# Optimization experiments

Measured on AMD Instinct MI355X. Metric: run time of the kernel, lower is better.

The kernel has to match this reference:

```python
import jax, jax.numpy as jnp
import numpy as np

N = 50000      # nodes
E = 800000     # edges (before self loops)
HID = 128      # hidden_dim
FEAT = 128     # feat_dim
NEG_SLOPE = 0.2
BN_EPS = 1e-5


def setup_inputs() -> dict:
    key = jax.random.key(0)
    ks = jax.random.split(key, 16)
    s = lambda d: 1.0 / np.sqrt(d).astype(np.float32)
    return {
        "x": jax.random.normal(ks[0], (N, HID), jnp.float32),
        "edge_index": jax.random.randint(ks[1], (2, E), 0, N, jnp.int32),
        # GATConv 1 (hidden -> hidden)
        "W1": jax.random.normal(ks[2], (HID, HID), jnp.float32) * s(HID),
        "att_src1": jax.random.normal(ks[3], (HID,), jnp.float32) * s(HID),
        "att_dst1": jax.random.normal(ks[4], (HID,), jnp.float32) * s(HID),
        "b1": jnp.zeros((HID,), jnp.float32),
        # BatchNorm1d(hidden) -- eval mode buffers/params
        "bn_gamma": jnp.ones((HID,), jnp.float32),
        "bn_beta": jnp.zeros((HID,), jnp.float32),
        "bn_mean": jax.random.normal(ks[5], (HID,), jnp.float32) * 0.1,
        "bn_var": jax.random.uniform(ks[6], (HID,), jnp.float32, 0.5, 1.5),
        # GATConv 2 (hidden -> feat)
        "W2": jax.random.normal(ks[7], (HID, FEAT), jnp.float32) * s(HID),
        "att_src2": jax.random.normal(ks[8], (FEAT,), jnp.float32) * s(FEAT),
        "att_dst2": jax.random.normal(ks[9], (FEAT,), jnp.float32) * s(FEAT),
        "b2": jnp.zeros((FEAT,), jnp.float32),
    }


def _gat_conv(x, W, att_src, att_dst, bias, src, dst, n_nodes):
    """PyG GATConv, heads=1: gather -> edge attn -> segment softmax -> scatter."""
    h = x @ W                                   # [N, d_out]
    a_s = h @ att_src                           # [N]
    a_d = h @ att_dst                           # [N]
    e = jax.nn.leaky_relu(a_s[src] + a_d[dst], NEG_SLOPE)  # [E']
    # numerically-stable softmax over incoming edges of each dst node
    e_max = jax.ops.segment_max(e, dst, num_segments=n_nodes)
    ex = jnp.exp(e - e_max[dst])
    denom = jax.ops.segment_sum(ex, dst, num_segments=n_nodes)
    alpha = ex / (denom[dst] + 1e-16)           # [E']
    out = jax.ops.segment_sum(alpha[:, None] * h[src], dst, num_segments=n_nodes)
    return out + bias


def reference(x, edge_index, W1, att_src1, att_dst1, b1,
              bn_gamma, bn_beta, bn_mean, bn_var,
              W2, att_src2, att_dst2, b2):
    n = x.shape[0]
    loops = jnp.arange(n, dtype=edge_index.dtype)
    src = jnp.concatenate([edge_index[0], loops])
    dst = jnp.concatenate([edge_index[1], loops])

    h = jax.nn.relu(_gat_conv(x, W1, att_src1, att_dst1, b1, src, dst, n))
    # BatchNorm1d in eval mode (running stats); dropout is identity in eval
    h = (h - bn_mean) * jax.lax.rsqrt(bn_var + BN_EPS) * bn_gamma + bn_beta
    out = jax.nn.relu(_gat_conv(h, W2, att_src2, att_dst2, b2, src, dst, n))
    return out
```

## Files before the change

### kernel.cpp

```cpp
#include <hip/hip_runtime.h>

typedef unsigned short u16;
typedef unsigned int   u32;

__device__ __forceinline__ float b2f(u16 h){ return __uint_as_float(((u32)h) << 16); }
__device__ __forceinline__ u16   f2b(float f){
  u32 u = __float_as_uint(f);
  u32 r = u + 0x7FFFu + ((u >> 16) & 1u);
  return (u16)(r >> 16);
}
__device__ __forceinline__ float lo16(u32 w){ return b2f((u16)(w & 0xFFFFu)); }
__device__ __forceinline__ float hi16(u32 w){ return b2f((u16)(w >> 16)); }

__global__ void r16_zero(int* p, int n){
  int t = blockIdx.x*blockDim.x + threadIdx.x;
  if (t < n) p[t] = 0;
}

__global__ void r16_hist(const int* ei, int E, int Ep, int* cnt){
  int t = blockIdx.x*blockDim.x + threadIdx.x;
  if (t >= Ep) return;
  int dst = (t < E) ? ei[E + t] : (t - E);
  atomicAdd(&cnt[dst], 1);
}

__global__ void r16_scan1(const int* in, int n, int* incl, int* bsums){
  __shared__ int tmp[256];
  int t = threadIdx.x; int g = blockIdx.x*256 + t;
  int v = (g < n) ? in[g] : 0;
  tmp[t] = v; __syncthreads();
  for (int off = 1; off < 256; off <<= 1){
    int u = (t >= off) ? tmp[t - off] : 0;
    __syncthreads();
    tmp[t] += u;
    __syncthreads();
  }
  if (g < n) incl[g] = tmp[t];
  if (t == 255) bsums[blockIdx.x] = tmp[255];
}

__global__ void r16_scan2(int* bsums, int nb){
  __shared__ int tmp[256];
  int t = threadIdx.x;
  int v = (t < nb) ? bsums[t] : 0;
  tmp[t] = v; __syncthreads();
  for (int off = 1; off < 256; off <<= 1){
    int u = (t >= off) ? tmp[t - off] : 0;
    __syncthreads();
    tmp[t] += u;
    __syncthreads();
  }
  if (t < nb) bsums[t] = tmp[t];
}

__global__ void r16_scan3(const int* incl, const int* cnt, const int* bsums,
                          int n, int Nnodes, int* offs, int* cursor){
  int t = threadIdx.x; int b = blockIdx.x; int g = b*256 + t;
  if (g >= n) return;
  int add = (b > 0) ? bsums[b-1] : 0;
  int ex = incl[g] - cnt[g] + add;
  offs[g] = ex;
  if (g < Nnodes) cursor[g] = ex;
}

__device__ __forceinline__ void r16_gemm_body(
    const float* __restrict__ X, const float* __restrict__ W,
    const float* __restrict__ atts, const float* __restrict__ attd,
    u16* __restrict__ HB, float* __restrict__ AS, float* __restrict__ AD,
    int nrows, int blk, float* xs){
  int t = threadIdx.x;
  int r0 = blk * 32;
  #pragma unroll
  for (int it = 0; it < 4; ++it){
    int idx = it*256 + t;
    int row = idx >> 5;
    int c4  = (idx & 31) * 4;
    float4 v = {0.f,0.f,0.f,0.f};
    if (r0 + row < nrows) v = *(const float4*)(X + (size_t)(r0+row)*128 + c4);
    *(float4*)&xs[row*128 + c4] = v;
  }
  __syncthreads();

  int cgrp = t & 31, rgrp = t >> 5;
  int col0 = cgrp * 4;
  float acc[4][4];
  #pragma unroll
  for (int r = 0; r < 4; ++r){
    #pragma unroll
    for (int j = 0; j < 4; ++j) acc[r][j] = 0.f;
  }
  #pragma unroll 2
  for (int k = 0; k < 128; k += 4){
    float4 w0 = *(const float4*)(W + (size_t)(k+0)*128 + col0);
    float4 w1 = *(const float4*)(W + (size_t)(k+1)*128 + col0);
    float4 w2 = *(const float4*)(W + (size_t)(k+2)*128 + col0);
    float4 w3 = *(const float4*)(W + (size_t)(k+3)*128 + col0);
    float4 xr[4];
    #pragma unroll
    for (int r = 0; r < 4; ++r) xr[r] = *(const float4*)&xs[(rgrp*4 + r)*128 + k];
    #pragma unroll
    for (int r = 0; r < 4; ++r){
      acc[r][0] = fmaf(xr[r].x, w0.x, acc[r][0]);
      acc[r][1] = fmaf(xr[r].x, w0.y, acc[r][1]);
      acc[r][2] = fmaf(xr[r].x, w0.z, acc[r][2]);
      acc[r][3] = fmaf(xr[r].x, w0.w, acc[r][3]);
      acc[r][0] = fmaf(xr[r].y, w1.x, acc[r][0]);
      acc[r][1] = fmaf(xr[r].y, w1.y, acc[r][1]);
      acc[r][2] = fmaf(xr[r].y, w1.z, acc[r][2]);
      acc[r][3] = fmaf(xr[r].y, w1.w, acc[r][3]);
      acc[r][0] = fmaf(xr[r].z, w2.x, acc[r][0]);
      acc[r][1] = fmaf(xr[r].z, w2.y, acc[r][1]);
      acc[r][2] = fmaf(xr[r].z, w2.z, acc[r][2]);
      acc[r][3] = fmaf(xr[r].z, w2.w, acc[r][3]);
      acc[r][0] = fmaf(xr[r].w, w3.x, acc[r][0]);
      acc[r][1] = fmaf(xr[r].w, w3.y, acc[r][1]);
      acc[r][2] = fmaf(xr[r].w, w3.z, acc[r][2]);
      acc[r][3] = fmaf(xr[r].w, w3.w, acc[r][3]);
    }
  }
  float4 sv = *(const float4*)(atts + col0);
  float4 dv = *(const float4*)(attd + col0);
  #pragma unroll
  for (int r = 0; r < 4; ++r){
    int row = r0 + rgrp*4 + r;
    float ps = acc[r][0]*sv.x + acc[r][1]*sv.y + acc[r][2]*sv.z + acc[r][3]*sv.w;
    float pd = acc[r][0]*dv.x + acc[r][1]*dv.y + acc[r][2]*dv.z + acc[r][3]*dv.w;
    #pragma unroll
    for (int off = 16; off >= 1; off >>= 1){
      ps += __shfl_xor(ps, off);
      pd += __shfl_xor(pd, off);
    }
    if (row < nrows){
      uint2 pb;
      pb.x = (u32)f2b(acc[r][0]) | ((u32)f2b(acc[r][1]) << 16);
      pb.y = (u32)f2b(acc[r][2]) | ((u32)f2b(acc[r][3]) << 16);
      *(uint2*)&HB[(size_t)row*128 + col0] = pb;
      if (cgrp == 0){ AS[row] = ps; AD[row] = pd; }
    }
  }
}

__global__ __launch_bounds__(256)
void r16_gemm_fill(const float* __restrict__ X, const float* __restrict__ W,
                   const float* __restrict__ atts, const float* __restrict__ attd,
                   u16* __restrict__ HB, float* __restrict__ AS, float* __restrict__ AD,
                   int nrows, int gemmBlocks,
                   const int* __restrict__ ei, int E, int Ep,
                   int* cursor, int* csr_src){
  __shared__ float xs[32*128];
  if ((int)blockIdx.x >= gemmBlocks){
    int g = ((int)blockIdx.x - gemmBlocks)*256 + threadIdx.x;
    if (g < Ep){
      int src, dst;
      if (g < E){ src = ei[g]; dst = ei[E + g]; } else { src = g - E; dst = g - E; }
      int pos = atomicAdd(&cursor[dst], 1);
      csr_src[pos] = src;
    }
    return;
  }
  r16_gemm_body(X, W, atts, attd, HB, AS, AD, nrows, blockIdx.x, xs);
}

__global__ __launch_bounds__(256)
void r16_gemm(const float* __restrict__ X, const float* __restrict__ W,
              const float* __restrict__ atts, const float* __restrict__ attd,
              u16* __restrict__ HB, float* __restrict__ AS, float* __restrict__ AD,
              int nrows){
  __shared__ float xs[32*128];
  r16_gemm_body(X, W, atts, attd, HB, AS, AD, nrows, blockIdx.x, xs);
}

__global__ __launch_bounds__(256)
void r16_aggregate(const u16* __restrict__ HB, const float* __restrict__ AS,
                   const float* __restrict__ AD,
                   const int* __restrict__ offs, const int* __restrict__ csr,
                   const float* __restrict__ bias,
                   const float* __restrict__ gamma_, const float* __restrict__ beta_,
                   const float* __restrict__ mean_, const float* __restrict__ var_,
                   float* __restrict__ outp, int n, int doBN){
  int wid  = (blockIdx.x*256 + threadIdx.x) >> 6;
  int lane = threadIdx.x & 63;
  if (wid >= n) return;
  int beg = offs[wid], end = offs[wid+1];
  int deg = end - beg;
  float ad = AD[wid];
  int c2 = lane*2;
  float a0 = 0.f, a1 = 0.f;

  if (deg <= 64){
    int   my_s = 0;
    float my_e = -3.0e38f;
    int myk = beg + lane;
    bool act = (myk < end);
    if (act){
      my_s = csr[myk];
      float e = AS[my_s] + ad;
      my_e = (e > 0.f) ? e : 0.2f*e;
    }
    float m = my_e;
    #pragma unroll
    for (int off = 32; off >= 1; off >>= 1) m = fmaxf(m, __shfl_xor(m, off));
    float pz = act ? __expf(my_e - m) : 0.f;
    float den = pz;
    #pragma unroll
    for (int off = 32; off >= 1; off >>= 1) den += __shfl_xor(den, off);
    float my_al = pz / (den + 1e-16f);

    int j = 0;
    for (; j + 8 <= deg; j += 8){
      int   s0 = __shfl(my_s, j),   s1 = __shfl(my_s, j+1);
      int   s2 = __shfl(my_s, j+2), s3 = __shfl(my_s, j+3);
      int   s4 = __shfl(my_s, j+4), s5 = __shfl(my_s, j+5);
      int   s6 = __shfl(my_s, j+6), s7 = __shfl(my_s, j+7);
      float l0 = __shfl(my_al, j),   l1 = __shfl(my_al, j+1);
      float l2 = __shfl(my_al, j+2), l3 = __shfl(my_al, j+3);
      float l4 = __shfl(my_al, j+4), l5 = __shfl(my_al, j+5);
      float l6 = __shfl(my_al, j+6), l7 = __shfl(my_al, j+7);
      u32 h0 = *(const u32*)&HB[(size_t)s0*128 + c2];
      u32 h1 = *(const u32*)&HB[(size_t)s1*128 + c2];
      u32 h2 = *(const u32*)&HB[(size_t)s2*128 + c2];
      u32 h3 = *(const u32*)&HB[(size_t)s3*128 + c2];
      u32 h4 = *(const u32*)&HB[(size_t)s4*128 + c2];
      u32 h5 = *(const u32*)&HB[(size_t)s5*128 + c2];
      u32 h6 = *(const u32*)&HB[(size_t)s6*128 + c2];
      u32 h7 = *(const u32*)&HB[(size_t)s7*128 + c2];
      a0 = fmaf(l0, lo16(h0), a0); a1 = fmaf(l0, hi16(h0), a1);
      a0 = fmaf(l1, lo16(h1), a0); a1 = fmaf(l1, hi16(h1), a1);
      a0 = fmaf(l2, lo16(h2), a0); a1 = fmaf(l2, hi16(h2), a1);
      a0 = fmaf(l3, lo16(h3), a0); a1 = fmaf(l3, hi16(h3), a1);
      a0 = fmaf(l4, lo16(h4), a0); a1 = fmaf(l4, hi16(h4), a1);
      a0 = fmaf(l5, lo16(h5), a0); a1 = fmaf(l5, hi16(h5), a1);
      a0 = fmaf(l6, lo16(h6), a0); a1 = fmaf(l6, hi16(h6), a1);
      a0 = fmaf(l7, lo16(h7), a0); a1 = fmaf(l7, hi16(h7), a1);
    }
    for (; j + 4 <= deg; j += 4){
      int   s0 = __shfl(my_s, j),   s1 = __shfl(my_s, j+1);
      int   s2 = __shfl(my_s, j+2), s3 = __shfl(my_s, j+3);
      float l0 = __shfl(my_al, j),   l1 = __shfl(my_al, j+1);
      float l2 = __shfl(my_al, j+2), l3 = __shfl(my_al, j+3);
      u32 h0 = *(const u32*)&HB[(size_t)s0*128 + c2];
      u32 h1 = *(const u32*)&HB[(size_t)s1*128 + c2];
      u32 h2 = *(const u32*)&HB[(size_t)s2*128 + c2];
      u32 h3 = *(const u32*)&HB[(size_t)s3*128 + c2];
      a0 = fmaf(l0, lo16(h0), a0); a1 = fmaf(l0, hi16(h0), a1);
      a0 = fmaf(l1, lo16(h1), a0); a1 = fmaf(l1, hi16(h1), a1);
      a0 = fmaf(l2, lo16(h2), a0); a1 = fmaf(l2, hi16(h2), a1);
      a0 = fmaf(l3, lo16(h3), a0); a1 = fmaf(l3, hi16(h3), a1);
    }
    for (; j < deg; ++j){
      int   s = __shfl(my_s, j);
      float l = __shfl(my_al, j);
      u32 hv = *(const u32*)&HB[(size_t)s*128 + c2];
      a0 = fmaf(l, lo16(hv), a0); a1 = fmaf(l, hi16(hv), a1);
    }
  } else {
    float m = -3.0e38f;
    for (int k = beg + lane; k < end; k += 64){
      int s = csr[k];
      float e = AS[s] + ad; e = (e > 0.f) ? e : 0.2f*e;
      m = fmaxf(m, e);
    }
    #pragma unroll
    for (int off = 32; off >= 1; off >>= 1) m = fmaxf(m, __shfl_xor(m, off));
    float den = 0.f;
    for (int k = beg + lane; k < end; k += 64){
      int s = csr[k];
      float e = AS[s] + ad; e = (e > 0.f) ? e : 0.2f*e;
      den += __expf(e - m);
    }
    #pragma unroll
    for (int off = 32; off >= 1; off >>= 1) den += __shfl_xor(den, off);
    float inv = 1.0f / (den + 1e-16f);
    for (int k = beg; k < end; ++k){
      int s = csr[k];
      float e = AS[s] + ad; e = (e > 0.f) ? e : 0.2f*e;
      float al = __expf(e - m) * inv;
      u32 hv = *(const u32*)&HB[(size_t)s*128 + c2];
      a0 = fmaf(al, lo16(hv), a0); a1 = fmaf(al, hi16(hv), a1);
    }
  }

  float v0 = a0 + bias[c2];
  float v1 = a1 + bias[c2+1];
  v0 = fmaxf(v0, 0.f); v1 = fmaxf(v1, 0.f);
  if (doBN){
    float s0 = gamma_[c2]   * rsqrtf(var_[c2]   + 1e-5f);
    float s1 = gamma_[c2+1] * rsqrtf(var_[c2+1] + 1e-5f);
    v0 = (v0 - mean_[c2])*s0   + beta_[c2];
    v1 = (v1 - mean_[c2+1])*s1 + beta_[c2+1];
  }
  float2 o = {v0, v1};
  ((float2*)(outp + (size_t)wid*128))[lane] = o;
}

extern "C" void kernel_launch(void* const* d_in, const int* in_sizes, int n_in,
                              void* d_out, int out_size, void* d_ws, size_t ws_size,
                              hipStream_t stream){
  const float* x   = (const float*)d_in[0];
  const int*   ei  = (const int*)  d_in[1];
  const float* W1  = (const float*)d_in[2];
  const float* as1 = (const float*)d_in[3];
  const float* ad1 = (const float*)d_in[4];
  const float* b1  = (const float*)d_in[5];
  const float* bng = (const float*)d_in[6];
  const float* bnb = (const float*)d_in[7];
  const float* bnm = (const float*)d_in[8];
  const float* bnv = (const float*)d_in[9];
  const float* W2  = (const float*)d_in[10];
  const float* as2 = (const float*)d_in[11];
  const float* ad2 = (const float*)d_in[12];
  const float* b2  = (const float*)d_in[13];
  float* out = (float*)d_out;

  int N  = in_sizes[0] / 128;
  int E  = in_sizes[1] / 2;
  int Ep = E + N;
  if (N <= 0 || E <= 0) return;

  char* base = (char*)d_ws;
  size_t off = 0;
  auto alloc = [&](size_t bytes)->char*{
    off = (off + 255) & ~(size_t)255;
    char* q = base + off; off += bytes; return q;
  };
  float* AS     = (float*)alloc((size_t)N*4);
  float* AD     = (float*)alloc((size_t)N*4);
  int*   cnt    = (int*)  alloc((size_t)(N+1)*4);
  int*   offs   = (int*)  alloc((size_t)(N+1)*4);
  int*   cursor = (int*)  alloc((size_t)N*4);
  int*   bsums  = (int*)  alloc(1024);
  int*   csr    = (int*)  alloc((size_t)Ep*4);
  u16*   hb     = (u16*)  alloc((size_t)N*128*2);
  float* x2     = (float*)alloc((size_t)N*128*4);

  int n1 = N + 1;
  int zb = (n1 + 255)/256;
  int eb = (Ep + 255)/256;
  int sb = (n1 + 255)/256;
  int gb = (N + 31)/32;
  int wb = (N + 3)/4;

  r16_zero <<<zb, 256, 0, stream>>>(cnt, n1);
  r16_hist <<<eb, 256, 0, stream>>>(ei, E, Ep, cnt);
  r16_scan1<<<sb, 256, 0, stream>>>(cnt, n1, offs, bsums);
  r16_scan2<<<1, 256, 0, stream>>>(bsums, sb);
  r16_scan3<<<sb, 256, 0, stream>>>(offs, cnt, bsums, n1, N, offs, cursor);

  r16_gemm_fill<<<gb + eb, 256, 0, stream>>>(x, W1, as1, ad1, hb, AS, AD, N, gb,
                                             ei, E, Ep, cursor, csr);
  r16_aggregate<<<wb, 256, 0, stream>>>(hb, AS, AD, offs, csr, b1, bng, bnb, bnm, bnv,
                                        x2, N, 1);
  r16_gemm     <<<gb, 256, 0, stream>>>(x2, W2, as2, ad2, hb, AS, AD, N);
  r16_aggregate<<<wb, 256, 0, stream>>>(hb, AS, AD, offs, csr, b2, 0, 0, 0, 0,
                                        out, N, 0);
}
```

Before: 313.1 us.

## Use bf16 MFMA for node feature GEMMs with pre-transposed bf16 weights

Replaces the scalar fp32 FMA GEMM with a 16x16x32 bf16 MFMA path. Each block now handles 64 rows, with X converted to bf16 and the pre-transposed bf16 W staged in padded shared memory. Two small prep kernels convert and transpose W1 and W2 each call. This targets the compute-bound dense projection; the costs are bf16 rounding of the X and W inputs, more shared memory per block, and narrower 16-bit scattered HB stores.

```diff
diff --git a/kernel.cpp b/kernel.cpp
--- a/kernel.cpp
+++ b/kernel.cpp
@@ -2,6 +2,8 @@
 
 typedef unsigned short u16;
 typedef unsigned int   u32;
+typedef short v8s __attribute__((ext_vector_type(8)));
+typedef float v4f __attribute__((ext_vector_type(4)));
 
 __device__ __forceinline__ float b2f(u16 h){ return __uint_as_float(((u32)h) << 16); }
 __device__ __forceinline__ u16   f2b(float f){
@@ -12,19 +14,22 @@
 __device__ __forceinline__ float lo16(u32 w){ return b2f((u16)(w & 0xFFFFu)); }
 __device__ __forceinline__ float hi16(u32 w){ return b2f((u16)(w >> 16)); }
 
-__global__ void r16_zero(int* p, int n){
+#define XS_STRIDE 136
+#define WS_STRIDE 136
+
+__global__ void r17_zero(int* p, int n){
   int t = blockIdx.x*blockDim.x + threadIdx.x;
   if (t < n) p[t] = 0;
 }
 
-__global__ void r16_hist(const int* ei, int E, int Ep, int* cnt){
+__global__ void r17_hist(const int* ei, int E, int Ep, int* cnt){
   int t = blockIdx.x*blockDim.x + threadIdx.x;
   if (t >= Ep) return;
   int dst = (t < E) ? ei[E + t] : (t - E);
   atomicAdd(&cnt[dst], 1);
 }
 
-__global__ void r16_scan1(const int* in, int n, int* incl, int* bsums){
+__global__ void r17_scan1(const int* in, int n, int* incl, int* bsums){
   __shared__ int tmp[256];
   int t = threadIdx.x; int g = blockIdx.x*256 + t;
   int v = (g < n) ? in[g] : 0;
@@ -39,7 +44,7 @@
   if (t == 255) bsums[blockIdx.x] = tmp[255];
 }
 
-__global__ void r16_scan2(int* bsums, int nb){
+__global__ void r17_scan2(int* bsums, int nb){
   __shared__ int tmp[256];
   int t = threadIdx.x;
   int v = (t < nb) ? bsums[t] : 0;
@@ -53,7 +58,7 @@
   if (t < nb) bsums[t] = tmp[t];
 }
 
-__global__ void r16_scan3(const int* incl, const int* cnt, const int* bsums,
+__global__ void r17_scan3(const int* incl, const int* cnt, const int* bsums,
                           int n, int Nnodes, int* offs, int* cursor){
   int t = threadIdx.x; int b = blockIdx.x; int g = b*256 + t;
   if (g >= n) return;
@@ -63,91 +68,96 @@
   if (g < Nnodes) cursor[g] = ex;
 }
 
-__device__ __forceinline__ void r16_gemm_body(
-    const float* __restrict__ X, const float* __restrict__ W,
+__global__ void r17_wprep(const float* __restrict__ W, u16* __restrict__ WT){
+  int t = blockIdx.x*256 + threadIdx.x;
+  int k = t >> 7, n = t & 127;
+  WT[n*128 + k] = f2b(W[k*128 + n]);
+}
+
+__device__ __forceinline__ void r17_gemm_body(
+    const float* __restrict__ X, const u16* __restrict__ WT,
     const float* __restrict__ atts, const float* __restrict__ attd,
     u16* __restrict__ HB, float* __restrict__ AS, float* __restrict__ AD,
-    int nrows, int blk, float* xs){
+    int nrows, int blk, u16* xs, u16* ws){
   int t = threadIdx.x;
-  int r0 = blk * 32;
-  #pragma unroll
-  for (int it = 0; it < 4; ++it){
+  int r0 = blk * 64;
+  #pragma unroll
+  for (int it = 0; it < 8; ++it){
     int idx = it*256 + t;
     int row = idx >> 5;
     int c4  = (idx & 31) * 4;
     float4 v = {0.f,0.f,0.f,0.f};
     if (r0 + row < nrows) v = *(const float4*)(X + (size_t)(r0+row)*128 + c4);
-    *(float4*)&xs[row*128 + c4] = v;
+    u16* d = &xs[row*XS_STRIDE + c4];
+    d[0]=f2b(v.x); d[1]=f2b(v.y); d[2]=f2b(v.z); d[3]=f2b(v.w);
+  }
+  #pragma unroll
+  for (int it = 0; it < 8; ++it){
+    int idx = it*256 + t;
+    int row = idx >> 4;
+    int c8  = (idx & 15) * 8;
+    *(uint4*)&ws[row*WS_STRIDE + c8] = *(const uint4*)&WT[row*128 + c8];
   }
   __syncthreads();
 
-  int cgrp = t & 31, rgrp = t >> 5;
-  int col0 = cgrp * 4;
-  float acc[4][4];
+  int wv   = t >> 6;
+  int lane = t & 63;
+  int m    = lane & 15;
+  int quad = lane >> 4;
+  int rw   = wv * 16;
+
+  v4f acc[8];
+  #pragma unroll
+  for (int ct = 0; ct < 8; ++ct) acc[ct] = (v4f){0.f,0.f,0.f,0.f};
+
+  #pragma unroll
+  for (int kb = 0; kb < 4; ++kb){
+    v8s a = *(const v8s*)&xs[(rw + m)*XS_STRIDE + kb*32 + quad*8];
+    #pragma unroll
+    for (int ct = 0; ct < 8; ++ct){
+      v8s b = *(const v8s*)&ws[(ct*16 + m)*WS_STRIDE + kb*32 + quad*8];
+      acc[ct] = __builtin_amdgcn_mfma_f32_16x16x32_bf16(a, b, acc[ct], 0, 0, 0);
+    }
+  }
+
+  float att_s[8], att_d[8];
+  #pragma unroll
+  for (int ct = 0; ct < 8; ++ct){
+    att_s[ct] = atts[ct*16 + m];
+    att_d[ct] = attd[ct*16 + m];
+  }
   #pragma unroll
   for (int r = 0; r < 4; ++r){
-    #pragma unroll
-    for (int j = 0; j < 4; ++j) acc[r][j] = 0.f;
-  }
-  #pragma unroll 2
-  for (int k = 0; k < 128; k += 4){
-    float4 w0 = *(const float4*)(W + (size_t)(k+0)*128 + col0);
-    float4 w1 = *(const float4*)(W + (size_t)(k+1)*128 + col0);
-    float4 w2 = *(const float4*)(W + (size_t)(k+2)*128 + col0);
-    float4 w3 = *(const float4*)(W + (size_t)(k+3)*128 + col0);
-    float4 xr[4];
-    #pragma unroll
-    for (int r = 0; r < 4; ++r) xr[r] = *(const float4*)&xs[(rgrp*4 + r)*128 + k];
-    #pragma unroll
-    for (int r = 0; r < 4; ++r){
-      acc[r][0] = fmaf(xr[r].x, w0.x, acc[r][0]);
-      acc[r][1] = fmaf(xr[r].x, w0.y, acc[r][1]);
-      acc[r][2] = fmaf(xr[r].x, w0.z, acc[r][2]);
-      acc[r][3] = fmaf(xr[r].x, w0.w, acc[r][3]);
-      acc[r][0] = fmaf(xr[r].y, w1.x, acc[r][0]);
-      acc[r][1] = fmaf(xr[r].y, w1.y, acc[r][1]);
-      acc[r][2] = fmaf(xr[r].y, w1.z, acc[r][2]);
-      acc[r][3] = fmaf(xr[r].y, w1.w, acc[r][3]);
-      acc[r][0] = fmaf(xr[r].z, w2.x, acc[r][0]);
-      acc[r][1] = fmaf(xr[r].z, w2.y, acc[r][1]);
-      acc[r][2] = fmaf(xr[r].z, w2.z, acc[r][2]);
-      acc[r][3] = fmaf(xr[r].z, w2.w, acc[r][3]);
-      acc[r][0] = fmaf(xr[r].w, w3.x, acc[r][0]);
-      acc[r][1] = fmaf(xr[r].w, w3.y, acc[r][1]);
-      acc[r][2] = fmaf(xr[r].w, w3.z, acc[r][2]);
-      acc[r][3] = fmaf(xr[r].w, w3.w, acc[r][3]);
-    }
-  }
-  float4 sv = *(const float4*)(atts + col0);
-  float4 dv = *(const float4*)(attd + col0);
-  #pragma unroll
-  for (int r = 0; r < 4; ++r){
-    int row = r0 + rgrp*4 + r;
-    float ps = acc[r][0]*sv.x + acc[r][1]*sv.y + acc[r][2]*sv.z + acc[r][3]*sv.w;
-    float pd = acc[r][0]*dv.x + acc[r][1]*dv.y + acc[r][2]*dv.z + acc[r][3]*dv.w;
-    #pragma unroll
-    for (int off = 16; off >= 1; off >>= 1){
+    int row = r0 + rw + quad*4 + r;
+    float ps = 0.f, pd = 0.f;
+    #pragma unroll
+    for (int ct = 0; ct < 8; ++ct){
+      ps = fmaf(acc[ct][r], att_s[ct], ps);
+      pd = fmaf(acc[ct][r], att_d[ct], pd);
+    }
+    #pragma unroll
+    for (int off = 8; off >= 1; off >>= 1){
       ps += __shfl_xor(ps, off);
       pd += __shfl_xor(pd, off);
     }
     if (row < nrows){
-      uint2 pb;
-      pb.x = (u32)f2b(acc[r][0]) | ((u32)f2b(acc[r][1]) << 16);
-      pb.y = (u32)f2b(acc[r][2]) | ((u32)f2b(acc[r][3]) << 16);
-      *(uint2*)&HB[(size_t)row*128 + col0] = pb;
-      if (cgrp == 0){ AS[row] = ps; AD[row] = pd; }
+      #pragma unroll
+      for (int ct = 0; ct < 8; ++ct)
+        HB[(size_t)row*128 + ct*16 + m] = f2b(acc[ct][r]);
+      if (m == 0){ AS[row] = ps; AD[row] = pd; }
     }
   }
 }
 
 __global__ __launch_bounds__(256)
-void r16_gemm_fill(const float* __restrict__ X, const float* __restrict__ W,
+void r17_gemm_fill(const float* __restrict__ X, const u16* __restrict__ WT,
                    const float* __restrict__ atts, const float* __restrict__ attd,
                    u16* __restrict__ HB, float* __restrict__ AS, float* __restrict__ AD,
                    int nrows, int gemmBlocks,
                    const int* __restrict__ ei, int E, int Ep,
                    int* cursor, int* csr_src){
-  __shared__ float xs[32*128];
+  __shared__ u16 xs[64*XS_STRIDE];
+  __shared__ u16 ws[128*WS_STRIDE];
   if ((int)blockIdx.x >= gemmBlocks){
     int g = ((int)blockIdx.x - gemmBlocks)*256 + threadIdx.x;
     if (g < Ep){
@@ -158,20 +168,21 @@
     }
     return;
   }
-  r16_gemm_body(X, W, atts, attd, HB, AS, AD, nrows, blockIdx.x, xs);
+  r17_gemm_body(X, WT, atts, attd, HB, AS, AD, nrows, blockIdx.x, xs, ws);
 }
 
 __global__ __launch_bounds__(256)
-void r16_gemm(const float* __restrict__ X, const float* __restrict__ W,
+void r17_gemm(const float* __restrict__ X, const u16* __restrict__ WT,
               const float* __restrict__ atts, const float* __restrict__ attd,
               u16* __restrict__ HB, float* __restrict__ AS, float* __restrict__ AD,
               int nrows){
-  __shared__ float xs[32*128];
-  r16_gemm_body(X, W, atts, attd, HB, AS, AD, nrows, blockIdx.x, xs);
+  __shared__ u16 xs[64*XS_STRIDE];
+  __shared__ u16 ws[128*WS_STRIDE];
+  r17_gemm_body(X, WT, atts, attd, HB, AS, AD, nrows, blockIdx.x, xs, ws);
 }
 
 __global__ __launch_bounds__(256)
-void r16_aggregate(const u16* __restrict__ HB, const float* __restrict__ AS,
+void r17_aggregate(const u16* __restrict__ HB, const float* __restrict__ AS,
                    const float* __restrict__ AD,
                    const int* __restrict__ offs, const int* __restrict__ csr,
                    const float* __restrict__ bias,
@@ -330,6 +341,8 @@
   int*   cursor = (int*)  alloc((size_t)N*4);
   int*   bsums  = (int*)  alloc(1024);
   int*   csr    = (int*)  alloc((size_t)Ep*4);
+  u16*   WT1    = (u16*)  alloc(16384*2);
+  u16*   WT2    = (u16*)  alloc(16384*2);
   u16*   hb     = (u16*)  alloc((size_t)N*128*2);
   float* x2     = (float*)alloc((size_t)N*128*4);
 
@@ -337,20 +350,22 @@
   int zb = (n1 + 255)/256;
   int eb = (Ep + 255)/256;
   int sb = (n1 + 255)/256;
-  int gb = (N + 31)/32;
+  int gb = (N + 63)/64;
   int wb = (N + 3)/4;
 
-  r16_zero <<<zb, 256, 0, stream>>>(cnt, n1);
-  r16_hist <<<eb, 256, 0, stream>>>(ei, E, Ep, cnt);
-  r16_scan1<<<sb, 256, 0, stream>>>(cnt, n1, offs, bsums);
-  r16_scan2<<<1, 256, 0, stream>>>(bsums, sb);
-  r16_scan3<<<sb, 256, 0, stream>>>(offs, cnt, bsums, n1, N, offs, cursor);
-
-  r16_gemm_fill<<<gb + eb, 256, 0, stream>>>(x, W1, as1, ad1, hb, AS, AD, N, gb,
+  r17_wprep<<<64, 256, 0, stream>>>(W1, WT1);
+  r17_wprep<<<64, 256, 0, stream>>>(W2, WT2);
+  r17_zero <<<zb, 256, 0, stream>>>(cnt, n1);
+  r17_hist <<<eb, 256, 0, stream>>>(ei, E, Ep, cnt);
+  r17_scan1<<<sb, 256, 0, stream>>>(cnt, n1, offs, bsums);
+  r17_scan2<<<1, 256, 0, stream>>>(bsums, sb);
+  r17_scan3<<<sb, 256, 0, stream>>>(offs, cnt, bsums, n1, N, offs, cursor);
+
+  r17_gemm_fill<<<gb + eb, 256, 0, stream>>>(x, WT1, as1, ad1, hb, AS, AD, N, gb,
                                              ei, E, Ep, cursor, csr);
-  r16_aggregate<<<wb, 256, 0, stream>>>(hb, AS, AD, offs, csr, b1, bng, bnb, bnm, bnv,
+  r17_aggregate<<<wb, 256, 0, stream>>>(hb, AS, AD, offs, csr, b1, bng, bnb, bnm, bnv,
                                         x2, N, 1);
-  r16_gemm     <<<gb, 256, 0, stream>>>(x2, W2, as2, ad2, hb, AS, AD, N);
-  r16_aggregate<<<wb, 256, 0, stream>>>(hb, AS, AD, offs, csr, b2, 0, 0, 0, 0,
+  r17_gemm     <<<gb, 256, 0, stream>>>(x2, WT2, as2, ad2, hb, AS, AD, N);
+  r17_aggregate<<<wb, 256, 0, stream>>>(hb, AS, AD, offs, csr, b2, 0, 0, 0, 0,
                                         out, N, 0);
 }
```

After: 310.7 us. Within noise of the previous version (-0.8%).
